# Performance work log

Hardware: AMD Instinct MI355X
Metric: run time of the kernel (lower is better)

The kernel has to match this reference:

```python
import jax, jax.numpy as jnp
import numpy as np

B, N0, E_PER, F_IN, NHID, NCLS = 128, 512, 2048, 128, 128, 2
RATIO = 0.5


def setup_inputs() -> dict:
    key = jax.random.key(0)
    ks = jax.random.split(key, 12)
    x = jax.random.normal(ks[0], (B * N0, F_IN), jnp.float32)
    # edges stay within each graph's contiguous node block (disconnected batched graphs)
    off = (jnp.arange(B, dtype=jnp.int32) * N0)[:, None]
    src = (jax.random.randint(ks[1], (B, E_PER), 0, N0, dtype=jnp.int32) + off).reshape(-1)
    dst = (jax.random.randint(ks[2], (B, E_PER), 0, N0, dtype=jnp.int32) + off).reshape(-1)

    def lin(k, fi, fo):
        return jax.random.normal(k, (fi, fo), jnp.float32) / np.sqrt(fi)

    return dict(
        x=x, src=src, dst=dst,
        W1=lin(ks[3], F_IN, NHID), b1=jnp.zeros((NHID,), jnp.float32),
        W2=lin(ks[4], NHID, NHID), b2=jnp.zeros((NHID,), jnp.float32),
        W3=lin(ks[5], NHID, NHID), b3=jnp.zeros((NHID,), jnp.float32),
        p1=jax.random.normal(ks[6], (NHID,), jnp.float32),
        p2=jax.random.normal(ks[7], (NHID,), jnp.float32),
        p3=jax.random.normal(ks[8], (NHID,), jnp.float32),
        L1=lin(ks[9], 2 * NHID, NHID), bl1=jnp.zeros((NHID,), jnp.float32),
        L2=lin(ks[10], NHID, NHID // 2), bl2=jnp.zeros((NHID // 2,), jnp.float32),
        L3=lin(ks[11], NHID // 2, NCLS), bl3=jnp.zeros((NCLS,), jnp.float32),
    )


def _gcn(x, src, dst, ew, W, b, n):
    h = x @ W
    deg = 1.0 + jax.ops.segment_sum(ew, dst, num_segments=n)  # self-loop contributes 1
    dinv = jax.lax.rsqrt(deg)
    msg = h[src] * (dinv[src] * dinv[dst] * ew)[:, None]
    return jax.ops.segment_sum(msg, dst, num_segments=n) + h * (dinv * dinv)[:, None] + b


def _topk_pool(x, pw, src, dst, ew, n_per):
    # TopKPooling: score = x.w/||w||; keep top ceil(ratio*n) nodes/graph; x' = x[perm]*tanh(score[perm])
    k = int(np.ceil(RATIO * n_per))
    score = x @ pw / jnp.linalg.norm(pw)
    _, loc = jax.lax.top_k(score.reshape(B, n_per), k)
    glob = (loc + (jnp.arange(B, dtype=loc.dtype) * n_per)[:, None]).reshape(-1)
    xk = x[glob] * jnp.tanh(score[glob])[:, None]
    # relabel kept nodes 0..B*k-1 (per-graph contiguous); mask edges touching dropped nodes
    new_id = jnp.full((B * n_per,), -1, jnp.int32).at[glob].set(jnp.arange(B * k, dtype=jnp.int32))
    ns, nd = new_id[src], new_id[dst]
    keep = (ns >= 0) & (nd >= 0)
    return xk, jnp.maximum(ns, 0), jnp.maximum(nd, 0), ew * keep.astype(ew.dtype), k


def _readout(x, k):
    # global_max_pool || global_mean_pool over each graph's k nodes
    xr = x.reshape(B, k, -1)
    return jnp.concatenate([xr.max(axis=1), xr.mean(axis=1)], axis=1)


def reference(x, src, dst, W1, b1, W2, b2, W3, b3, p1, p2, p3, L1, bl1, L2, bl2, L3, bl3):
    src = src.astype(jnp.int32)
    dst = dst.astype(jnp.int32)
    ew = jnp.ones(src.shape, x.dtype)
    h = jax.nn.relu(_gcn(x, src, dst, ew, W1, b1, B * N0))
    h, s1, d1, ew, k1 = _topk_pool(h, p1, src, dst, ew, N0)
    r1 = _readout(h, k1)
    h = jax.nn.relu(_gcn(h, s1, d1, ew, W2, b2, B * k1))
    h, s2, d2, ew, k2 = _topk_pool(h, p2, s1, d1, ew, k1)
    r2 = _readout(h, k2)
    h = jax.nn.relu(_gcn(h, s2, d2, ew, W3, b3, B * k2))
    h, s3, d3, ew, k3 = _topk_pool(h, p3, s2, d2, ew, k2)
    r3 = _readout(h, k3)
    z = r1 + r2 + r3
    z = jax.nn.relu(z @ L1 + bl1)  # dropout: eval mode, identity
    z = jax.nn.relu(z @ L2 + bl2)
    return jax.nn.log_softmax(z @ L3 + bl3, axis=-1)
```

## Files before the change

kernel.cpp:

```cpp
#include <hip/hip_runtime.h>
#include <math.h>

#define NB 128
#define E_PER 2048
#define NE (NB * E_PER)
#define FD 128

__global__ __launch_bounds__(256) void gemm64(const float* __restrict__ A,
                                              const float* __restrict__ W,
                                              float* __restrict__ C,
                                              int swz_shift) {
    const int bid = blockIdx.x;
    const int xcd = bid & 7;
    const int q = bid >> 3;
    const int S = swz_shift;
    const int tile = ((q >> S) << (3 + S)) | (xcd << S) | (q & ((1 << S) - 1));

    __shared__ float At[32 * 68];
    __shared__ float Wt[32 * 128];
    const int tid = threadIdx.x;
    const long rbase = (long)tile * 64;
    const int cg = tid & 15;
    const int rg = tid >> 4;

    float acc[2][4][4];
#pragma unroll
    for (int b = 0; b < 2; ++b)
#pragma unroll
        for (int i = 0; i < 4; ++i)
#pragma unroll
            for (int j = 0; j < 4; ++j) acc[b][i][j] = 0.f;

    for (int k0 = 0; k0 < 128; k0 += 32) {
        __syncthreads();
#pragma unroll
        for (int qq = 0; qq < 2; ++qq) {
            int idx = tid + 256 * qq;
            int row = idx >> 3, kq = idx & 7;
            float4 a = *(const float4*)&A[(rbase + row) * FD + k0 + kq * 4];
            At[(kq * 4 + 0) * 68 + row] = a.x;
            At[(kq * 4 + 1) * 68 + row] = a.y;
            At[(kq * 4 + 2) * 68 + row] = a.z;
            At[(kq * 4 + 3) * 68 + row] = a.w;
        }
#pragma unroll
        for (int qq = 0; qq < 4; ++qq) {
            int idx = tid + 256 * qq;
            int kk = idx >> 5, cq = idx & 31;
            *(float4*)&Wt[kk * 128 + cq * 4] =
                *(const float4*)&W[(k0 + kk) * FD + cq * 4];
        }
        __syncthreads();
#pragma unroll 8
        for (int kk = 0; kk < 32; ++kk) {
            float4 a  = *(const float4*)&At[kk * 68 + rg * 4];
            float4 b0 = *(const float4*)&Wt[kk * 128 + cg * 4];
            float4 b1 = *(const float4*)&Wt[kk * 128 + 64 + cg * 4];
            float av[4] = {a.x, a.y, a.z, a.w};
            float bv[2][4] = {{b0.x, b0.y, b0.z, b0.w}, {b1.x, b1.y, b1.z, b1.w}};
#pragma unroll
            for (int b = 0; b < 2; ++b)
#pragma unroll
                for (int i = 0; i < 4; ++i)
#pragma unroll
                    for (int j = 0; j < 4; ++j)
                        acc[b][i][j] += av[i] * bv[b][j];
        }
    }
#pragma unroll
    for (int i = 0; i < 4; ++i) {
        long row = rbase + rg * 4 + i;
#pragma unroll
        for (int b = 0; b < 2; ++b) {
            float4 o = {acc[b][i][0], acc[b][i][1], acc[b][i][2], acc[b][i][3]};
            *(float4*)&C[row * FD + b * 64 + cg * 4] = o;
        }
    }
}

__global__ __launch_bounds__(256) void build_csr(const int* __restrict__ src,
                                                 const int* __restrict__ dst,
                                                 const float* __restrict__ ew,
                                                 int n_per,
                                                 float* __restrict__ dinv,
                                                 int* __restrict__ roff,
                                                 float2* __restrict__ cpair) {
    __shared__ int   cnt[512];
    __shared__ int   offs[513];
    __shared__ float dl[512];
    const int g = blockIdx.x, tid = threadIdx.x;
    const int ebase = g * E_PER;
    const int nbase = g * n_per;

    for (int i = tid; i < n_per; i += 256) cnt[i] = 0;
    __syncthreads();
    for (int i = tid; i < E_PER; i += 256) {
        float w = ew ? ew[ebase + i] : 1.0f;
        if (w != 0.f) atomicAdd(&cnt[dst[ebase + i] - nbase], 1);
    }
    __syncthreads();
    for (int i = tid; i < n_per; i += 256) {
        float di = rsqrtf(1.0f + (float)cnt[i]);
        dl[i] = di;
        dinv[nbase + i] = di;
    }
    __syncthreads();
    if (tid == 0) {
        int run = 0;
        for (int i = 0; i < n_per; ++i) { offs[i] = run; run += cnt[i]; }
        offs[n_per] = run;
    }
    __syncthreads();
    for (int i = tid; i <= n_per; i += 256)
        roff[g * (n_per + 1) + i] = ebase + offs[i];
    for (int i = tid; i < n_per; i += 256) cnt[i] = offs[i];
    __syncthreads();
    for (int i = tid; i < E_PER; i += 256) {
        float w = ew ? ew[ebase + i] : 1.0f;
        if (w != 0.f) {
            int s = src[ebase + i], d = dst[ebase + i];
            int dlo = d - nbase;
            int pos = atomicAdd(&cnt[dlo], 1);
            cpair[ebase + pos] = make_float2(__int_as_float(s), dl[s - nbase] * dl[dlo] * w);
        }
    }
}

__global__ __launch_bounds__(256) void agg_csr(const float* __restrict__ hpre,
                                               const int* __restrict__ roff,
                                               const float2* __restrict__ cpair,
                                               const float* __restrict__ dinv,
                                               const float* __restrict__ bias,
                                               const float* __restrict__ pvec,
                                               int np_shift,
                                               float* __restrict__ hout,
                                               float* __restrict__ scraw) {
    const int tid = threadIdx.x;
    const int P = 1 << (np_shift - 2);
    const int xcd = blockIdx.x & 7;
    const int idx = blockIdx.x >> 3;
    const int p = idx & (P - 1);
    const int g = ((idx >> (np_shift - 2)) << 3) + xcd;
    const int n_per = 1 << np_shift;
    const int nl = p * 4 + (tid >> 6);
    const int node = g * n_per + nl;
    const int l = tid & 63;
    const float2* __restrict__ hpre2 = (const float2*)hpre;
    const int rbase = g * (n_per + 1) + nl;
    const int e0 = roff[rbase], e1 = roff[rbase + 1];
    const float2 selfh = hpre2[(long)node * 64 + l];
    float ax = 0.f, ay = 0.f;
    int e = e0, n = e1 - e0;
    while (n >= 4) {
        float2 p0 = cpair[e], p1 = cpair[e + 1], p2 = cpair[e + 2], p3 = cpair[e + 3];
        float2 h0 = hpre2[(long)__float_as_int(p0.x) * 64 + l];
        float2 h1 = hpre2[(long)__float_as_int(p1.x) * 64 + l];
        float2 h2 = hpre2[(long)__float_as_int(p2.x) * 64 + l];
        float2 h3 = hpre2[(long)__float_as_int(p3.x) * 64 + l];
        ax += h0.x * p0.y + h1.x * p1.y + h2.x * p2.y + h3.x * p3.y;
        ay += h0.y * p0.y + h1.y * p1.y + h2.y * p2.y + h3.y * p3.y;
        e += 4; n -= 4;
    }
    while (n > 0) {
        float2 pr = cpair[e];
        float2 hv = hpre2[(long)__float_as_int(pr.x) * 64 + l];
        ax += hv.x * pr.y;
        ay += hv.y * pr.y;
        ++e; --n;
    }
    const float di = dinv[node];
    const float d2 = di * di;
    const float2 bb = ((const float2*)bias)[l];
    float v0 = fmaxf(ax + selfh.x * d2 + bb.x, 0.f);
    float v1 = fmaxf(ay + selfh.y * d2 + bb.y, 0.f);
    ((float2*)hout)[(long)node * 64 + l] = make_float2(v0, v1);

    const float2 pv = ((const float2*)pvec)[l];
    float pr = v0 * pv.x + v1 * pv.y;
#pragma unroll
    for (int o = 32; o > 0; o >>= 1) pr += __shfl_down(pr, o);
    if (l == 0) scraw[node] = pr;
}

__global__ __launch_bounds__(512) void pool_kernel(const float* __restrict__ h,
                                                   const float* __restrict__ scraw,
                                                   const float* __restrict__ p,
                                                   int n_per, int k,
                                                   float* __restrict__ xp,
                                                   int* __restrict__ newid,
                                                   float* __restrict__ rout) {
    __shared__ float sc[512];
    __shared__ int   ord[256];
    __shared__ float tf[256];
    __shared__ float red[128];
    __shared__ float mxs[512];
    __shared__ float sms[512];
    const int tid = threadIdx.x;
    const int g = blockIdx.x;
    const int nbase = g * n_per;

    if (tid < 128) { float pv = p[tid]; red[tid] = pv * pv; }
    __syncthreads();
    for (int s = 64; s > 0; s >>= 1) {
        if (tid < s) red[tid] += red[tid + s];
        __syncthreads();
    }
    const float invn = rsqrtf(red[0]);

    if (tid < n_per) sc[tid] = scraw[nbase + tid] * invn;
    __syncthreads();

    if (tid < n_per) {
        const float si = sc[tid];
        int rank = 0;
        for (int j = 0; j < n_per; ++j) {
            float sj = sc[j];
            rank += (sj > si) || (sj == si && j < tid);
        }
        if (rank < k) {
            ord[rank] = tid;
            tf[rank] = tanhf(si);
            newid[nbase + tid] = g * k + rank;
        } else {
            newid[nbase + tid] = -1;
        }
    }
    __syncthreads();

    const int f = tid & 127;
    const int grp = tid >> 7;
    float mx = -INFINITY, sm = 0.f;
    for (int t = tid; t < k * FD; t += 512) {
        int r = t >> 7;
        float val = h[(long)(nbase + ord[r]) * FD + f] * tf[r];
        xp[((long)g * k + r) * FD + f] = val;
        mx = fmaxf(mx, val);
        sm += val;
    }
    mxs[grp * 128 + f] = mx;
    sms[grp * 128 + f] = sm;
    __syncthreads();
    if (tid < 128) {
        float m0 = fmaxf(fmaxf(mxs[f], mxs[128 + f]), fmaxf(mxs[256 + f], mxs[384 + f]));
        float s0 = sms[f] + sms[128 + f] + sms[256 + f] + sms[384 + f];
        rout[g * 256 + f] = m0;
        rout[g * 256 + 128 + f] = s0 / (float)k;
    }
}

__global__ __launch_bounds__(256) void relabel_kernel(const int* __restrict__ src,
                                                      const int* __restrict__ dst,
                                                      const float* __restrict__ ew,
                                                      const int* __restrict__ newid,
                                                      int* __restrict__ nsrc,
                                                      int* __restrict__ ndst,
                                                      float* __restrict__ new_ew) {
    const int e = blockIdx.x * 256 + threadIdx.x;
    int s = src[e], d = dst[e];
    float w = ew ? ew[e] : 1.0f;
    int ns = newid[s], nd = newid[d];
    bool keep = (ns >= 0) && (nd >= 0);
    nsrc[e] = ns > 0 ? ns : 0;
    ndst[e] = nd > 0 ? nd : 0;
    new_ew[e] = keep ? w : 0.f;
}

__global__ __launch_bounds__(128) void mlp_kernel(const float* __restrict__ r1,
                                                  const float* __restrict__ r2,
                                                  const float* __restrict__ r3,
                                                  const float* __restrict__ L1,
                                                  const float* __restrict__ bl1,
                                                  const float* __restrict__ L2,
                                                  const float* __restrict__ bl2,
                                                  const float* __restrict__ L3,
                                                  const float* __restrict__ bl3,
                                                  float* __restrict__ out) {
    __shared__ float z[256], z1[128], z2[64];
    const int g = blockIdx.x, tid = threadIdx.x;
    for (int t = tid; t < 256; t += 128)
        z[t] = r1[g * 256 + t] + r2[g * 256 + t] + r3[g * 256 + t];
    __syncthreads();
    {
        float a = bl1[tid];
        for (int i = 0; i < 256; ++i) a += z[i] * L1[i * 128 + tid];
        z1[tid] = fmaxf(a, 0.f);
    }
    __syncthreads();
    if (tid < 64) {
        float a = bl2[tid];
        for (int i = 0; i < 128; ++i) a += z1[i] * L2[i * 64 + tid];
        z2[tid] = fmaxf(a, 0.f);
    }
    __syncthreads();
    if (tid == 0) {
        float l0 = bl3[0], l1v = bl3[1];
        for (int i = 0; i < 64; ++i) {
            l0  += z2[i] * L3[i * 2 + 0];
            l1v += z2[i] * L3[i * 2 + 1];
        }
        float m = fmaxf(l0, l1v);
        float lse = m + logf(expf(l0 - m) + expf(l1v - m));
        out[g * 2 + 0] = l0 - lse;
        out[g * 2 + 1] = l1v - lse;
    }
}

extern "C" void kernel_launch(void* const* d_in, const int* in_sizes, int n_in,
                              void* d_out, int out_size, void* d_ws, size_t ws_size,
                              hipStream_t stream) {
    const float* x   = (const float*)d_in[0];
    const int*  src0 = (const int*)d_in[1];
    const int*  dst0 = (const int*)d_in[2];
    const float* W1 = (const float*)d_in[3];  const float* b1  = (const float*)d_in[4];
    const float* W2 = (const float*)d_in[5];  const float* b2  = (const float*)d_in[6];
    const float* W3 = (const float*)d_in[7];  const float* b3  = (const float*)d_in[8];
    const float* p1 = (const float*)d_in[9];  const float* p2  = (const float*)d_in[10];
    const float* p3 = (const float*)d_in[11];
    const float* L1 = (const float*)d_in[12]; const float* bl1 = (const float*)d_in[13];
    const float* L2 = (const float*)d_in[14]; const float* bl2 = (const float*)d_in[15];
    const float* L3 = (const float*)d_in[16]; const float* bl3 = (const float*)d_in[17];
    float* out = (float*)d_out;

    char* wptr = (char*)d_ws;
    auto alloc = [&](size_t bytes) {
        char* r = wptr;
        wptr += (bytes + 255) & ~(size_t)255;
        return r;
    };
    float* hpre = (float*)alloc(65536ULL * FD * 4);
    float* hbuf = (float*)alloc(65536ULL * FD * 4);
    float* xp2  = (float*)alloc(32768ULL * FD * 4);
    float* xp3  = (float*)alloc(16384ULL * FD * 4);
    float* xp4  = (float*)alloc(8192ULL * FD * 4);
    float* dinv = (float*)alloc(65536ULL * 4);
    float* scraw= (float*)alloc(65536ULL * 4);
    int*   nid  = (int*)alloc(65536ULL * 4);
    int*   src1 = (int*)alloc(NE * 4);
    int*   dst1 = (int*)alloc(NE * 4);
    float* ew1  = (float*)alloc(NE * 4);
    int*   src2 = (int*)alloc(NE * 4);
    int*   dst2 = (int*)alloc(NE * 4);
    float* ew2  = (float*)alloc(NE * 4);
    int*   roff = (int*)alloc((size_t)NB * 513 * 4);
    float2* cpair = (float2*)alloc((size_t)NE * 8);
    float* r1   = (float*)alloc(128ULL * 256 * 4);
    float* r2   = (float*)alloc(128ULL * 256 * 4);
    float* r3   = (float*)alloc(128ULL * 256 * 4);

    gemm64<<<1024, 256, 0, stream>>>(x, W1, hpre, 3);
    build_csr<<<NB, 256, 0, stream>>>(src0, dst0, nullptr, 512, dinv, roff, cpair);
    agg_csr<<<65536 / 4, 256, 0, stream>>>(hpre, roff, cpair, dinv, b1, p1, 9, hbuf, scraw);
    pool_kernel<<<NB, 512, 0, stream>>>(hbuf, scraw, p1, 512, 256, xp2, nid, r1);
    relabel_kernel<<<NE / 256, 256, 0, stream>>>(src0, dst0, nullptr, nid, src1, dst1, ew1);

    gemm64<<<512, 256, 0, stream>>>(xp2, W2, hpre, 2);
    build_csr<<<NB, 256, 0, stream>>>(src1, dst1, ew1, 256, dinv, roff, cpair);
    agg_csr<<<32768 / 4, 256, 0, stream>>>(hpre, roff, cpair, dinv, b2, p2, 8, hbuf, scraw);
    pool_kernel<<<NB, 512, 0, stream>>>(hbuf, scraw, p2, 256, 128, xp3, nid, r2);
    relabel_kernel<<<NE / 256, 256, 0, stream>>>(src1, dst1, ew1, nid, src2, dst2, ew2);

    gemm64<<<256, 256, 0, stream>>>(xp3, W3, hpre, 1);
    build_csr<<<NB, 256, 0, stream>>>(src2, dst2, ew2, 128, dinv, roff, cpair);
    agg_csr<<<16384 / 4, 256, 0, stream>>>(hpre, roff, cpair, dinv, b3, p3, 7, hbuf, scraw);
    pool_kernel<<<NB, 512, 0, stream>>>(hbuf, scraw, p3, 128, 64, xp4, nid, r3);

    mlp_kernel<<<NB, 128, 0, stream>>>(r1, r2, r3, L1, bl1, L2, bl2, L3, bl3, out);
}
```

Before: 344.1 us.

## Fold edge relabeling into CSR build via composed node maps; widen pool blocks

The separate relabel kernels are removed. build_csr now reads the original edge lists and maps each endpoint through the stored per-level newid tables, composing two maps for the third level. Edges with a dropped endpoint are skipped, so no edge-weight array is needed. This saves two launches and the write and re-read of the relabeled src, dst and weight arrays, at the cost of extra gather lookups inside build_csr. Separately, pool_kernel moves from 512 to 1024 threads per block, with an 8-way final reduction, to spread the gather and readout work over more threads.

```diff
diff --git a/kernel.cpp b/kernel.cpp
--- a/kernel.cpp
+++ b/kernel.cpp
@@ -80,7 +80,8 @@
 
 __global__ __launch_bounds__(256) void build_csr(const int* __restrict__ src,
                                                  const int* __restrict__ dst,
-                                                 const float* __restrict__ ew,
+                                                 const int* __restrict__ map1,
+                                                 const int* __restrict__ map2,
                                                  int n_per,
                                                  float* __restrict__ dinv,
                                                  int* __restrict__ roff,
@@ -92,11 +93,18 @@
     const int ebase = g * E_PER;
     const int nbase = g * n_per;
 
+    auto mapid = [&](int v) -> int {
+        if (map1) { v = map1[v]; if (v < 0) return -1; }
+        if (map2) { v = map2[v]; }
+        return v;
+    };
+
     for (int i = tid; i < n_per; i += 256) cnt[i] = 0;
     __syncthreads();
     for (int i = tid; i < E_PER; i += 256) {
-        float w = ew ? ew[ebase + i] : 1.0f;
-        if (w != 0.f) atomicAdd(&cnt[dst[ebase + i] - nbase], 1);
+        int ms = mapid(src[ebase + i]);
+        int md = mapid(dst[ebase + i]);
+        if (ms >= 0 && md >= 0) atomicAdd(&cnt[md - nbase], 1);
     }
     __syncthreads();
     for (int i = tid; i < n_per; i += 256) {
@@ -116,12 +124,12 @@
     for (int i = tid; i < n_per; i += 256) cnt[i] = offs[i];
     __syncthreads();
     for (int i = tid; i < E_PER; i += 256) {
-        float w = ew ? ew[ebase + i] : 1.0f;
-        if (w != 0.f) {
-            int s = src[ebase + i], d = dst[ebase + i];
-            int dlo = d - nbase;
+        int ms = mapid(src[ebase + i]);
+        int md = mapid(dst[ebase + i]);
+        if (ms >= 0 && md >= 0) {
+            int dlo = md - nbase;
             int pos = atomicAdd(&cnt[dlo], 1);
-            cpair[ebase + pos] = make_float2(__int_as_float(s), dl[s - nbase] * dl[dlo] * w);
+            cpair[ebase + pos] = make_float2(__int_as_float(ms), dl[ms - nbase] * dl[dlo]);
         }
     }
 }
@@ -182,19 +190,19 @@
     if (l == 0) scraw[node] = pr;
 }
 
-__global__ __launch_bounds__(512) void pool_kernel(const float* __restrict__ h,
-                                                   const float* __restrict__ scraw,
-                                                   const float* __restrict__ p,
-                                                   int n_per, int k,
-                                                   float* __restrict__ xp,
-                                                   int* __restrict__ newid,
-                                                   float* __restrict__ rout) {
+__global__ __launch_bounds__(1024) void pool_kernel(const float* __restrict__ h,
+                                                    const float* __restrict__ scraw,
+                                                    const float* __restrict__ p,
+                                                    int n_per, int k,
+                                                    float* __restrict__ xp,
+                                                    int* __restrict__ newid,
+                                                    float* __restrict__ rout) {
     __shared__ float sc[512];
     __shared__ int   ord[256];
     __shared__ float tf[256];
     __shared__ float red[128];
-    __shared__ float mxs[512];
-    __shared__ float sms[512];
+    __shared__ float mxs[1024];
+    __shared__ float sms[1024];
     const int tid = threadIdx.x;
     const int g = blockIdx.x;
     const int nbase = g * n_per;
@@ -230,7 +238,7 @@
     const int f = tid & 127;
     const int grp = tid >> 7;
     float mx = -INFINITY, sm = 0.f;
-    for (int t = tid; t < k * FD; t += 512) {
+    for (int t = tid; t < k * FD; t += 1024) {
         int r = t >> 7;
         float val = h[(long)(nbase + ord[r]) * FD + f] * tf[r];
         xp[((long)g * k + r) * FD + f] = val;
@@ -241,28 +249,15 @@
     sms[grp * 128 + f] = sm;
     __syncthreads();
     if (tid < 128) {
-        float m0 = fmaxf(fmaxf(mxs[f], mxs[128 + f]), fmaxf(mxs[256 + f], mxs[384 + f]));
-        float s0 = sms[f] + sms[128 + f] + sms[256 + f] + sms[384 + f];
+        float m0 = mxs[f], s0 = sms[f];
+#pragma unroll
+        for (int q = 1; q < 8; ++q) {
+            m0 = fmaxf(m0, mxs[q * 128 + f]);
+            s0 += sms[q * 128 + f];
+        }
         rout[g * 256 + f] = m0;
         rout[g * 256 + 128 + f] = s0 / (float)k;
     }
-}
-
-__global__ __launch_bounds__(256) void relabel_kernel(const int* __restrict__ src,
-                                                      const int* __restrict__ dst,
-                                                      const float* __restrict__ ew,
-                                                      const int* __restrict__ newid,
-                                                      int* __restrict__ nsrc,
-                                                      int* __restrict__ ndst,
-                                                      float* __restrict__ new_ew) {
-    const int e = blockIdx.x * 256 + threadIdx.x;
-    int s = src[e], d = dst[e];
-    float w = ew ? ew[e] : 1.0f;
-    int ns = newid[s], nd = newid[d];
-    bool keep = (ns >= 0) && (nd >= 0);
-    nsrc[e] = ns > 0 ? ns : 0;
-    ndst[e] = nd > 0 ? nd : 0;
-    new_ew[e] = keep ? w : 0.f;
 }
 
 __global__ __launch_bounds__(128) void mlp_kernel(const float* __restrict__ r1,
@@ -334,13 +329,9 @@
     float* xp4  = (float*)alloc(8192ULL * FD * 4);
     float* dinv = (float*)alloc(65536ULL * 4);
     float* scraw= (float*)alloc(65536ULL * 4);
-    int*   nid  = (int*)alloc(65536ULL * 4);
-    int*   src1 = (int*)alloc(NE * 4);
-    int*   dst1 = (int*)alloc(NE * 4);
-    float* ew1  = (float*)alloc(NE * 4);
-    int*   src2 = (int*)alloc(NE * 4);
-    int*   dst2 = (int*)alloc(NE * 4);
-    float* ew2  = (float*)alloc(NE * 4);
+    int*   nid1 = (int*)alloc(65536ULL * 4);
+    int*   nid2 = (int*)alloc(32768ULL * 4);
+    int*   nid3 = (int*)alloc(16384ULL * 4);
     int*   roff = (int*)alloc((size_t)NB * 513 * 4);
     float2* cpair = (float2*)alloc((size_t)NE * 8);
     float* r1   = (float*)alloc(128ULL * 256 * 4);
@@ -348,21 +339,19 @@
     float* r3   = (float*)alloc(128ULL * 256 * 4);
 
     gemm64<<<1024, 256, 0, stream>>>(x, W1, hpre, 3);
-    build_csr<<<NB, 256, 0, stream>>>(src0, dst0, nullptr, 512, dinv, roff, cpair);
+    build_csr<<<NB, 256, 0, stream>>>(src0, dst0, nullptr, nullptr, 512, dinv, roff, cpair);
     agg_csr<<<65536 / 4, 256, 0, stream>>>(hpre, roff, cpair, dinv, b1, p1, 9, hbuf, scraw);
-    pool_kernel<<<NB, 512, 0, stream>>>(hbuf, scraw, p1, 512, 256, xp2, nid, r1);
-    relabel_kernel<<<NE / 256, 256, 0, stream>>>(src0, dst0, nullptr, nid, src1, dst1, ew1);
+    pool_kernel<<<NB, 1024, 0, stream>>>(hbuf, scraw, p1, 512, 256, xp2, nid1, r1);
 
     gemm64<<<512, 256, 0, stream>>>(xp2, W2, hpre, 2);
-    build_csr<<<NB, 256, 0, stream>>>(src1, dst1, ew1, 256, dinv, roff, cpair);
+    build_csr<<<NB, 256, 0, stream>>>(src0, dst0, nid1, nullptr, 256, dinv, roff, cpair);
     agg_csr<<<32768 / 4, 256, 0, stream>>>(hpre, roff, cpair, dinv, b2, p2, 8, hbuf, scraw);
-    pool_kernel<<<NB, 512, 0, stream>>>(hbuf, scraw, p2, 256, 128, xp3, nid, r2);
-    relabel_kernel<<<NE / 256, 256, 0, stream>>>(src1, dst1, ew1, nid, src2, dst2, ew2);
+    pool_kernel<<<NB, 1024, 0, stream>>>(hbuf, scraw, p2, 256, 128, xp3, nid2, r2);
 
     gemm64<<<256, 256, 0, stream>>>(xp3, W3, hpre, 1);
-    build_csr<<<NB, 256, 0, stream>>>(src2, dst2, ew2, 128, dinv, roff, cpair);
+    build_csr<<<NB, 256, 0, stream>>>(src0, dst0, nid1, nid2, 128, dinv, roff, cpair);
     agg_csr<<<16384 / 4, 256, 0, stream>>>(hpre, roff, cpair, dinv, b3, p3, 7, hbuf, scraw);
-    pool_kernel<<<NB, 512, 0, stream>>>(hbuf, scraw, p3, 128, 64, xp4, nid, r3);
+    pool_kernel<<<NB, 1024, 0, stream>>>(hbuf, scraw, p3, 128, 64, xp4, nid3, r3);
 
     mlp_kernel<<<NB, 128, 0, stream>>>(r1, r2, r3, L1, bl1, L2, bl2, L3, bl3, out);
 }
```

New measurement: 331.2 us. 1.04x faster.
